# Kernel tuning notes

Hardware: AMD Instinct MI355X
Metric: run time of the kernel (lower is better)

The kernel has to match this reference:

```python
import jax, jax.numpy as jnp
import numpy as np

B, N, C = 64, 1024, 128
H1, H2 = 256, 128
ACTION = N


def _xavier(key, shape):
    lim = float(np.sqrt(6.0 / (shape[0] + shape[1])))
    return jax.random.uniform(key, shape, jnp.float32, -lim, lim)


def setup_inputs() -> dict:
    key = jax.random.key(0)
    ks = jax.random.split(key, 16)
    node_features = jax.random.normal(ks[0], (B, N, 3), jnp.float32)
    adjacency_matrix = jax.random.randint(ks[1], (B, N, N), 0, 2).astype(jnp.int32)
    return {
        "node_features": node_features,
        "adjacency_matrix": adjacency_matrix,
        "W_in": _xavier(ks[2], (3, C)),
        "a_src": _xavier(ks[3], (C, 1)),
        "a_dst": _xavier(ks[4], (C, 1)),
        "a_src2": _xavier(ks[5], (C, 1)),
        "a_dst2": _xavier(ks[6], (C, 1)),
        "W1": _xavier(ks[7], (C, H1)),
        "b1": jnp.zeros((H1,), jnp.float32),
        "W2": _xavier(ks[8], (H1, H2)),
        "b2": jnp.zeros((H2,), jnp.float32),
        "Wpi": _xavier(ks[9], (H2, ACTION)),
        "bpi": jnp.zeros((ACTION,), jnp.float32),
        "Wv": _xavier(ks[10], (H2, 1)),
        "bv": jnp.zeros((1,), jnp.float32),
    }


def _gat_layer(x, mask, a_src, a_dst):
    # x: [B,N,C]; mask: [B,N,N] bool
    ai = jnp.squeeze(x @ a_src, -1)  # [B,N] score of node as source (i)
    aj = jnp.squeeze(x @ a_dst, -1)  # [B,N] score of node as dest (j)
    e = ai[:, :, None] + aj[:, None, :]  # [B,N,N]
    e = jnp.where(e > 0, e, 0.2 * e)  # leaky_relu(0.2)
    e = jnp.where(mask, e, jnp.float32(-1e9))  # masked_fill(-inf)
    alpha = jax.nn.softmax(e, axis=-1)  # [B,N,N]
    out = jnp.einsum("bij,bjc->bic", alpha, x)  # weighted neighbor aggregation
    return jax.nn.relu(out)


def reference(node_features, adjacency_matrix, W_in, a_src, a_dst, a_src2, a_dst2,
              W1, b1, W2, b2, Wpi, bpi, Wv, bv):
    mask = adjacency_matrix > 0
    x = node_features @ W_in  # [B,N,C], no bias
    x = _gat_layer(x, mask, a_src, a_dst)
    x = _gat_layer(x, mask, a_src2, a_dst2)
    x = jnp.mean(x, axis=1)  # [B,C]
    x = jax.nn.relu(x @ W1 + b1)
    x = jax.nn.relu(x @ W2 + b2)
    pi = jax.nn.softmax(x @ Wpi + bpi, axis=1)
    v = x @ Wv + bv
    return (pi, v)
```

## Files before the change

### kernel.cpp

```cpp
#include <hip/hip_runtime.h>

#define Bn 64
#define Nn 1024
#define Cc 128

typedef _Float16 h8 __attribute__((ext_vector_type(8)));
typedef float f4v __attribute__((ext_vector_type(4)));
typedef unsigned long long u64;

__global__ __launch_bounds__(256) void k_feat(
    const float* __restrict__ nf, const float* __restrict__ Win,
    const float* __restrict__ asrc, const float* __restrict__ adst,
    _Float16* __restrict__ X0, float* __restrict__ ai, float* __restrict__ aj,
    float* __restrict__ E, float* __restrict__ G, float* __restrict__ F, float* __restrict__ H) {
  int g = blockIdx.x; int b = g >> 7; int n0 = (g & 127) << 3;
  int t = threadIdx.x; int c = t >> 1; int h = t & 1;
  __shared__ float sNf[24];
  if (t < 24) sNf[t] = nf[((size_t)(b << 10) + n0) * 3 + t];
  float w0 = Win[c], w1 = Win[Cc + c], w2 = Win[2 * Cc + c];
  float as_ = asrc[c], ad = adst[c];
  __syncthreads();
  float ps[4], pd[4];
  _Float16 hv[4];
  #pragma unroll
  for (int r = 0; r < 4; r++) {
    const float* p = sNf + ((h << 2) + r) * 3;
    float x = p[0] * w0 + p[1] * w1 + p[2] * w2;
    hv[r] = (_Float16)x; ps[r] = x * as_; pd[r] = x * ad;
  }
  *(uint2*)(X0 + ((size_t)b << 17) + ((size_t)(g & 127) << 10) + (c << 3) + (h << 2)) = *(uint2*)hv;
  #pragma unroll
  for (int off = 32; off > 1; off >>= 1) {
    #pragma unroll
    for (int r = 0; r < 4; r++) { ps[r] += __shfl_down(ps[r], off, 64); pd[r] += __shfl_down(pd[r], off, 64); }
  }
  __shared__ float red[4][2][4][2];
  int lane = t & 63, wv = t >> 6;
  if (lane < 2) {
    #pragma unroll
    for (int r = 0; r < 4; r++) { red[wv][lane][r][0] = ps[r]; red[wv][lane][r][1] = pd[r]; }
  }
  __syncthreads();
  if (t < 8) {
    int hh = t >> 2, r = t & 3;
    float sa = 0.f, sd = 0.f;
    #pragma unroll
    for (int w = 0; w < 4; w++) { sa += red[w][hh][r][0]; sd += red[w][hh][r][1]; }
    int gi = (b << 10) + n0 + t;
    ai[gi] = sa; aj[gi] = sd;
    E[gi] = __expf(sa); G[gi] = __expf(0.2f * sa);
    F[gi] = __expf(sd); H[gi] = __expf(0.2f * sd);
  }
}

template <int LAYER>
__global__ __launch_bounds__(256, 3) void k_agg(
    const _Float16* __restrict__ X, const int* __restrict__ adj,
    const float* __restrict__ ai, const float* __restrict__ E, const float* __restrict__ G,
    const float* __restrict__ aj, const float* __restrict__ F, const float* __restrict__ H,
    u64* __restrict__ pm, _Float16* __restrict__ Y, float* __restrict__ xmp,
    const float* __restrict__ as2, const float* __restrict__ ad2,
    float* __restrict__ ai2o, float* __restrict__ aj2o,
    float* __restrict__ E2o, float* __restrict__ G2o,
    float* __restrict__ F2o, float* __restrict__ H2o) {
  __shared__ __align__(16) char smem[34816];
  float* s_aj = (float*)smem;
  float* s_F  = (float*)(smem + 4096);
  float* s_H  = (float*)(smem + 8192);
  unsigned char* s_pm = (unsigned char*)(smem + 12288);
  float* tile = (float*)smem;
  float* s_as2 = (float*)(smem + 33792);
  float* s_ad2 = (float*)(smem + 34304);

  const int lin = blockIdx.x;
  const int b = lin & 63, tile_id = lin >> 6, i0 = tile_id << 6;
  const int tid = threadIdx.x;
  const int lane = tid & 63, wv = tid >> 6;
  const int m = lane & 15, quad = lane >> 4;
  const int wi = wv >> 1, wc = wv & 1;
  const int gbase = b << 10;

  ((float4*)s_aj)[tid] = ((const float4*)(aj + gbase))[tid];
  ((float4*)s_F)[tid]  = ((const float4*)(F + gbase))[tid];
  ((float4*)s_H)[tid]  = ((const float4*)(H + gbase))[tid];
  if (LAYER == 1 && tid < 128) { s_as2[tid] = as2[tid]; s_ad2[tid] = ad2[tid]; }

  if (LAYER == 1) {
    ushort* pmu = (ushort*)pm;
    #pragma unroll 2
    for (int pass = 0; pass < 16; ++pass) {
      int r = (wv << 4) + pass;
      const uint4* arow = (const uint4*)(adj + ((size_t)(gbase + i0 + r) << 10));
      uint4 v0 = arow[(lane << 2) | 0], v1 = arow[(lane << 2) | 1];
      uint4 v2 = arow[(lane << 2) | 2], v3 = arow[(lane << 2) | 3];
      unsigned int bits =
          (v0.x) | (v0.y << 1) | (v0.z << 2) | (v0.w << 3) |
          (v1.x << 4) | (v1.y << 5) | (v1.z << 6) | (v1.w << 7) |
          (v2.x << 8) | (v2.y << 9) | (v2.z << 10) | (v2.w << 11) |
          (v3.x << 12) | (v3.y << 13) | (v3.z << 14) | (v3.w << 15);
      *(ushort*)(s_pm + r * 152 + (lane << 1)) = (ushort)bits;
      pmu[((size_t)(gbase + i0 + r) << 6) + lane] = (ushort)bits;
    }
  } else {
    const u64* pmg = pm + (((size_t)(gbase + i0)) << 4);
    #pragma unroll
    for (int k = tid; k < 1024; k += 256) {
      int r = k >> 4, w = k & 15;
      *(u64*)(s_pm + r * 152 + (w << 3)) = pmg[k];
    }
  }

  const int r0 = (wi << 5) + m;
  const int gi0 = gbase + i0 + r0;
  const float ai0 = ai[gi0],      E0c = E[gi0],      G0c = G[gi0];
  const float ai1 = ai[gi0 + 16], E1c = E[gi0 + 16], G1c = G[gi0 + 16];
  float dsum0 = 0.f, dsum1 = 0.f;

  f4v acc[2][4];
  #pragma unroll
  for (int a = 0; a < 2; a++)
    #pragma unroll
    for (int ct = 0; ct < 4; ct++) { f4v z = {0.f, 0.f, 0.f, 0.f}; acc[a][ct] = z; }

  const char* gB = (const char*)(X + ((size_t)b << 17)) + (((quad << 7) + (wc << 6) + m) << 4);
  const unsigned char* pmr0 = s_pm + r0 * 152;
  const unsigned char* pmr1 = pmr0 + 16 * 152;

  auto LOADK = [&](int kt, h8& B0, h8& B1, h8& B2, h8& B3,
                   float4& W0, float4& W1, float4& Fw0, float4& Fw1,
                   float4& Hw0, float4& Hw1, unsigned& M0, unsigned& M1) {
    const char* gp = gB + ((size_t)kt << 13);
    B0 = *(const h8*)gp;          B1 = *(const h8*)(gp + 256);
    B2 = *(const h8*)(gp + 512);  B3 = *(const h8*)(gp + 768);
    const int j0 = (kt << 5) + (quad << 3);
    W0  = *(const float4*)&s_aj[j0]; W1  = *(const float4*)&s_aj[j0 + 4];
    Fw0 = *(const float4*)&s_F[j0];  Fw1 = *(const float4*)&s_F[j0 + 4];
    Hw0 = *(const float4*)&s_H[j0];  Hw1 = *(const float4*)&s_H[j0 + 4];
    M0 = pmr0[(kt << 2) + quad];     M1 = pmr1[(kt << 2) + quad];
  };
  auto COMP = [&](h8 B0, h8 B1, h8 B2, h8 B3,
                  float4 W0, float4 W1, float4 Fw0, float4 Fw1,
                  float4 Hw0, float4 Hw1, unsigned M0, unsigned M1) {
    float aw[8], fw[8], hw[8];
    *(float4*)&aw[0] = W0;  *(float4*)&aw[4] = W1;
    *(float4*)&fw[0] = Fw0; *(float4*)&fw[4] = Fw1;
    *(float4*)&hw[0] = Hw0; *(float4*)&hw[4] = Hw1;
    h8 a0, a1;
    #pragma unroll
    for (int e = 0; e < 8; e++) {
      float ew = aw[e], fe = fw[e], he = hw[e];
      bool p0 = (ai0 + ew) > 0.f;
      float v0 = (p0 ? E0c : G0c) * (p0 ? fe : he);
      v0 = ((M0 >> e) & 1u) ? v0 : 0.f;
      dsum0 += v0; a0[e] = (_Float16)v0;
      bool p1 = (ai1 + ew) > 0.f;
      float v1 = (p1 ? E1c : G1c) * (p1 ? fe : he);
      v1 = ((M1 >> e) & 1u) ? v1 : 0.f;
      dsum1 += v1; a1[e] = (_Float16)v1;
    }
    acc[0][0] = __builtin_amdgcn_mfma_f32_16x16x32_f16(a0, B0, acc[0][0], 0, 0, 0);
    acc[1][0] = __builtin_amdgcn_mfma_f32_16x16x32_f16(a1, B0, acc[1][0], 0, 0, 0);
    acc[0][1] = __builtin_amdgcn_mfma_f32_16x16x32_f16(a0, B1, acc[0][1], 0, 0, 0);
    acc[1][1] = __builtin_amdgcn_mfma_f32_16x16x32_f16(a1, B1, acc[1][1], 0, 0, 0);
    acc[0][2] = __builtin_amdgcn_mfma_f32_16x16x32_f16(a0, B2, acc[0][2], 0, 0, 0);
    acc[1][2] = __builtin_amdgcn_mfma_f32_16x16x32_f16(a1, B2, acc[1][2], 0, 0, 0);
    acc[0][3] = __builtin_amdgcn_mfma_f32_16x16x32_f16(a0, B3, acc[0][3], 0, 0, 0);
    acc[1][3] = __builtin_amdgcn_mfma_f32_16x16x32_f16(a1, B3, acc[1][3], 0, 0, 0);
  };

  __syncthreads();

  h8 Ab0, Ab1, Ab2, Ab3; float4 Aw0, Aw1, Af0, Af1, Ah0, Ah1; unsigned Am0, Am1;
  h8 Bb0, Bb1, Bb2, Bb3; float4 Bw0, Bw1, Bf0, Bf1, Bh0, Bh1; unsigned Bm0, Bm1;
  LOADK(0, Ab0, Ab1, Ab2, Ab3, Aw0, Aw1, Af0, Af1, Ah0, Ah1, Am0, Am1);
  for (int kt = 0; kt < 32; kt += 2) {
    LOADK(kt + 1, Bb0, Bb1, Bb2, Bb3, Bw0, Bw1, Bf0, Bf1, Bh0, Bh1, Bm0, Bm1);
    COMP(Ab0, Ab1, Ab2, Ab3, Aw0, Aw1, Af0, Af1, Ah0, Ah1, Am0, Am1);
    LOADK(kt + 2, Ab0, Ab1, Ab2, Ab3, Aw0, Aw1, Af0, Af1, Ah0, Ah1, Am0, Am1);
    COMP(Bb0, Bb1, Bb2, Bb3, Bw0, Bw1, Bf0, Bf1, Bh0, Bh1, Bm0, Bm1);
  }

  dsum0 += __shfl_xor(dsum0, 16, 64);
  dsum0 += __shfl_xor(dsum0, 32, 64);
  dsum1 += __shfl_xor(dsum1, 16, 64);
  dsum1 += __shfl_xor(dsum1, 32, 64);
  float rd8[2][4];
  #pragma unroll
  for (int r = 0; r < 4; r++) {
    int src = (quad << 2) + r;
    rd8[0][r] = 1.0f / __shfl(dsum0, src, 64);
    rd8[1][r] = 1.0f / __shfl(dsum1, src, 64);
  }

  __syncthreads();
  #pragma unroll
  for (int a = 0; a < 2; a++)
    #pragma unroll
    for (int ct = 0; ct < 4; ct++)
      #pragma unroll
      for (int r = 0; r < 4; r++) {
        int lr = (wi << 5) + (a << 4) + (quad << 2) + r;
        int c = (wc << 6) + (ct << 4) + m;
        tile[lr * 132 + c] = fmaxf(acc[a][ct][r] * rd8[a][r], 0.f);
      }
  __syncthreads();
  if (LAYER == 1) {
    _Float16 hv[32];
    #pragma unroll
    for (int s = 0; s < 32; s++) {
      int q = (tid << 5) + s;
      int li = ((q >> 10) << 3) + (q & 7), c = (q >> 3) & 127;
      hv[s] = (_Float16)tile[li * 132 + c];
    }
    uint4* o = (uint4*)(Y + ((size_t)b << 17) + ((size_t)i0 << 7) + (tid << 5));
    o[0] = *(uint4*)&hv[0]; o[1] = *(uint4*)&hv[8];
    o[2] = *(uint4*)&hv[16]; o[3] = *(uint4*)&hv[24];
    {
      int i = tid >> 2, p = tid & 3, cb = p << 5;
      const float* trow = tile + i * 132 + cb;
      float ssrc = 0.f, sdst = 0.f;
      #pragma unroll
      for (int k = 0; k < 32; k += 4) {
        float4 tv = *(const float4*)(trow + k);
        float4 av = *(const float4*)(s_as2 + cb + k);
        float4 dv = *(const float4*)(s_ad2 + cb + k);
        ssrc += tv.x * av.x + tv.y * av.y + tv.z * av.z + tv.w * av.w;
        sdst += tv.x * dv.x + tv.y * dv.y + tv.z * dv.z + tv.w * dv.w;
      }
      ssrc += __shfl_xor(ssrc, 1, 64); ssrc += __shfl_xor(ssrc, 2, 64);
      sdst += __shfl_xor(sdst, 1, 64); sdst += __shfl_xor(sdst, 2, 64);
      int gi = gbase + i0 + i;
      if (p == 0) { ai2o[gi] = ssrc; E2o[gi] = __expf(ssrc); G2o[gi] = __expf(0.2f * ssrc); }
      else if (p == 1) { aj2o[gi] = sdst; F2o[gi] = __expf(sdst); H2o[gi] = __expf(0.2f * sdst); }
    }
  } else {
    if (tid < 128) {
      float s = 0.f;
      #pragma unroll
      for (int i = 0; i < 64; i++) s += tile[i * 132 + tid];
      xmp[(((b << 4) + tile_id) << 7) + tid] = s;
    }
  }
}

__global__ __launch_bounds__(256) void k_head(
    const float* __restrict__ xmp, const float* __restrict__ W1, const float* __restrict__ b1,
    const float* __restrict__ W2, const float* __restrict__ b2,
    const float* __restrict__ Wpi, const float* __restrict__ bpi,
    const float* __restrict__ Wv, const float* __restrict__ bv,
    float* __restrict__ out) {
  int b = blockIdx.x, t = threadIdx.x;
  __shared__ float xs[128], h1[256], h2[128], red[4];
  if (t < 128) {
    const float* p = xmp + ((size_t)b << 11);
    float s = 0.f;
    #pragma unroll
    for (int xb = 0; xb < 16; xb++) s += p[(xb << 7) + t];
    xs[t] = s * (1.f / 1024.f);
  }
  __syncthreads();
  float s = 0.f;
  #pragma unroll 8
  for (int k = 0; k < 128; k++) s += xs[k] * W1[k * 256 + t];
  h1[t] = fmaxf(s + b1[t], 0.f);
  __syncthreads();
  if (t < 128) {
    float s2 = 0.f;
    #pragma unroll 8
    for (int k = 0; k < 256; k++) s2 += h1[k] * W2[k * 128 + t];
    h2[t] = fmaxf(s2 + b2[t], 0.f);
  }
  __syncthreads();
  float lg[4];
  #pragma unroll
  for (int q = 0; q < 4; q++) {
    int o = t + (q << 8);
    float s3 = 0.f;
    #pragma unroll 8
    for (int k = 0; k < 128; k++) s3 += h2[k] * Wpi[k * 1024 + o];
    lg[q] = s3 + bpi[o];
  }
  float mx = fmaxf(fmaxf(lg[0], lg[1]), fmaxf(lg[2], lg[3]));
  #pragma unroll
  for (int off = 32; off > 0; off >>= 1) mx = fmaxf(mx, __shfl_down(mx, off, 64));
  if ((t & 63) == 0) red[t >> 6] = mx;
  __syncthreads();
  mx = fmaxf(fmaxf(red[0], red[1]), fmaxf(red[2], red[3]));
  __syncthreads();
  float ex[4]; float sum = 0.f;
  #pragma unroll
  for (int q = 0; q < 4; q++) { ex[q] = __expf(lg[q] - mx); sum += ex[q]; }
  #pragma unroll
  for (int off = 32; off > 0; off >>= 1) sum += __shfl_down(sum, off, 64);
  if ((t & 63) == 0) red[t >> 6] = sum;
  __syncthreads();
  sum = red[0] + red[1] + red[2] + red[3];
  float rs = 1.0f / sum;
  #pragma unroll
  for (int q = 0; q < 4; q++) out[((size_t)b << 10) + t + (q << 8)] = ex[q] * rs;
  __syncthreads();
  float vp = (t < 128) ? h2[t] * Wv[t] : 0.f;
  #pragma unroll
  for (int off = 32; off > 0; off >>= 1) vp += __shfl_down(vp, off, 64);
  if ((t & 63) == 0) red[t >> 6] = vp;
  __syncthreads();
  if (t == 0) out[65536 + b] = red[0] + red[1] + red[2] + red[3] + bv[0];
}

extern "C" void kernel_launch(void* const* d_in, const int* in_sizes, int n_in,
                              void* d_out, int out_size, void* d_ws, size_t ws_size,
                              hipStream_t stream) {
  const float* nf    = (const float*)d_in[0];
  const int*   adj   = (const int*)  d_in[1];
  const float* Win   = (const float*)d_in[2];
  const float* asrc  = (const float*)d_in[3];
  const float* adst  = (const float*)d_in[4];
  const float* asrc2 = (const float*)d_in[5];
  const float* adst2 = (const float*)d_in[6];
  const float* W1    = (const float*)d_in[7];
  const float* b1    = (const float*)d_in[8];
  const float* W2    = (const float*)d_in[9];
  const float* b2    = (const float*)d_in[10];
  const float* Wpi   = (const float*)d_in[11];
  const float* bpi   = (const float*)d_in[12];
  const float* Wv    = (const float*)d_in[13];
  const float* bv    = (const float*)d_in[14];
  float* out = (float*)d_out;

  char* ws = (char*)d_ws;
  _Float16* x0 = (_Float16*)(ws);
  _Float16* x1 = (_Float16*)(ws + 16777216);
  u64* pm = (u64*)(ws + 33554432);
  char* S = ws + 41943040;
  float* ai1 = (float*)(S + 0 * 262144);
  float* aj1 = (float*)(S + 1 * 262144);
  float* E1  = (float*)(S + 2 * 262144);
  float* G1  = (float*)(S + 3 * 262144);
  float* F1  = (float*)(S + 4 * 262144);
  float* H1  = (float*)(S + 5 * 262144);
  float* ai2 = (float*)(S + 6 * 262144);
  float* aj2 = (float*)(S + 7 * 262144);
  float* E2  = (float*)(S + 8 * 262144);
  float* G2  = (float*)(S + 9 * 262144);
  float* F2  = (float*)(S + 10 * 262144);
  float* H2  = (float*)(S + 11 * 262144);
  float* xmp = (float*)(S + 12 * 262144);

  k_feat<<<8192, 256, 0, stream>>>(nf, Win, asrc, adst, x0, ai1, aj1, E1, G1, F1, H1);
  k_agg<1><<<1024, 256, 0, stream>>>(x0, adj, ai1, E1, G1, aj1, F1, H1, pm, x1, nullptr,
                                     asrc2, adst2, ai2, aj2, E2, G2, F2, H2);
  k_agg<2><<<1024, 256, 0, stream>>>(x1, nullptr, ai2, E2, G2, aj2, F2, H2, pm, nullptr, xmp,
                                     nullptr, nullptr, nullptr, nullptr, nullptr, nullptr, nullptr, nullptr);
  k_head<<<Bn, 256, 0, stream>>>(xmp, W1, b1, W2, b2, Wpi, bpi, Wv, bv, out);
}
```

Baseline: 564.6 us.

## Move adjacency bitpacking into feature kernel and simplify GAT softmax weights

Adjacency bit-packing moves out of layer-1 aggregation and into the feature kernel, which is much more parallel, so both aggregation layers now read the packed mask the same way. The leaky-relu branch is replaced by max(E*F, G*H), which is valid because exp is monotonic, so the ai/aj arrays and their comparisons are dropped. The mask is applied with bitwise AND on packed fp16 pairs. Row denominators are now computed with an extra MFMA against a ones vector instead of scalar sums and shuffles. Occupancy hint rises from 3 to 4 waves; risks include register pressure and fp16 rounding in the denominators.

Result: faster. 505.3 us (-10.5%).

```diff
diff --git a/kernel.cpp b/kernel.cpp
--- a/kernel.cpp
+++ b/kernel.cpp
@@ -5,16 +5,18 @@
 #define Cc 128
 
 typedef _Float16 h8 __attribute__((ext_vector_type(8)));
+typedef __fp16 fp16x2 __attribute__((ext_vector_type(2)));
 typedef float f4v __attribute__((ext_vector_type(4)));
 typedef unsigned long long u64;
 
 __global__ __launch_bounds__(256) void k_feat(
     const float* __restrict__ nf, const float* __restrict__ Win,
     const float* __restrict__ asrc, const float* __restrict__ adst,
-    _Float16* __restrict__ X0, float* __restrict__ ai, float* __restrict__ aj,
+    const int* __restrict__ adj, _Float16* __restrict__ X0, u64* __restrict__ pm,
     float* __restrict__ E, float* __restrict__ G, float* __restrict__ F, float* __restrict__ H) {
   int g = blockIdx.x; int b = g >> 7; int n0 = (g & 127) << 3;
   int t = threadIdx.x; int c = t >> 1; int h = t & 1;
+  int lane = t & 63, wv = t >> 6;
   __shared__ float sNf[24];
   if (t < 24) sNf[t] = nf[((size_t)(b << 10) + n0) * 3 + t];
   float w0 = Win[c], w1 = Win[Cc + c], w2 = Win[2 * Cc + c];
@@ -29,13 +31,31 @@
     hv[r] = (_Float16)x; ps[r] = x * as_; pd[r] = x * ad;
   }
   *(uint2*)(X0 + ((size_t)b << 17) + ((size_t)(g & 127) << 10) + (c << 3) + (h << 2)) = *(uint2*)hv;
+
+  {
+    ushort* pmu = (ushort*)pm;
+    int row = n0 + (wv << 1);
+    const uint4* ar = (const uint4*)(adj + (((size_t)(b << 10) + row) << 10));
+    #pragma unroll
+    for (int rr = 0; rr < 2; rr++) {
+      uint4 v0 = ar[(lane << 2) | 0], v1 = ar[(lane << 2) | 1];
+      uint4 v2 = ar[(lane << 2) | 2], v3 = ar[(lane << 2) | 3];
+      unsigned int bits =
+          (v0.x) | (v0.y << 1) | (v0.z << 2) | (v0.w << 3) |
+          (v1.x << 4) | (v1.y << 5) | (v1.z << 6) | (v1.w << 7) |
+          (v2.x << 8) | (v2.y << 9) | (v2.z << 10) | (v2.w << 11) |
+          (v3.x << 12) | (v3.y << 13) | (v3.z << 14) | (v3.w << 15);
+      pmu[(((size_t)(b << 10) + row + rr) << 6) + lane] = (ushort)bits;
+      ar += 256;
+    }
+  }
+
   #pragma unroll
   for (int off = 32; off > 1; off >>= 1) {
     #pragma unroll
     for (int r = 0; r < 4; r++) { ps[r] += __shfl_down(ps[r], off, 64); pd[r] += __shfl_down(pd[r], off, 64); }
   }
   __shared__ float red[4][2][4][2];
-  int lane = t & 63, wv = t >> 6;
   if (lane < 2) {
     #pragma unroll
     for (int r = 0; r < 4; r++) { red[wv][lane][r][0] = ps[r]; red[wv][lane][r][1] = pd[r]; }
@@ -47,27 +67,24 @@
     #pragma unroll
     for (int w = 0; w < 4; w++) { sa += red[w][hh][r][0]; sd += red[w][hh][r][1]; }
     int gi = (b << 10) + n0 + t;
-    ai[gi] = sa; aj[gi] = sd;
     E[gi] = __expf(sa); G[gi] = __expf(0.2f * sa);
     F[gi] = __expf(sd); H[gi] = __expf(0.2f * sd);
   }
 }
 
 template <int LAYER>
-__global__ __launch_bounds__(256, 3) void k_agg(
-    const _Float16* __restrict__ X, const int* __restrict__ adj,
-    const float* __restrict__ ai, const float* __restrict__ E, const float* __restrict__ G,
-    const float* __restrict__ aj, const float* __restrict__ F, const float* __restrict__ H,
-    u64* __restrict__ pm, _Float16* __restrict__ Y, float* __restrict__ xmp,
+__global__ __launch_bounds__(256, 4) void k_agg(
+    const _Float16* __restrict__ X,
+    const float* __restrict__ E, const float* __restrict__ G,
+    const float* __restrict__ F, const float* __restrict__ H,
+    const u64* __restrict__ pm, _Float16* __restrict__ Y, float* __restrict__ xmp,
     const float* __restrict__ as2, const float* __restrict__ ad2,
-    float* __restrict__ ai2o, float* __restrict__ aj2o,
     float* __restrict__ E2o, float* __restrict__ G2o,
     float* __restrict__ F2o, float* __restrict__ H2o) {
   __shared__ __align__(16) char smem[34816];
-  float* s_aj = (float*)smem;
-  float* s_F  = (float*)(smem + 4096);
-  float* s_H  = (float*)(smem + 8192);
-  unsigned char* s_pm = (unsigned char*)(smem + 12288);
+  float* s_F  = (float*)smem;
+  float* s_H  = (float*)(smem + 4096);
+  unsigned char* s_pm = (unsigned char*)(smem + 8192);
   float* tile = (float*)smem;
   float* s_as2 = (float*)(smem + 33792);
   float* s_ad2 = (float*)(smem + 34304);
@@ -80,117 +97,99 @@
   const int wi = wv >> 1, wc = wv & 1;
   const int gbase = b << 10;
 
-  ((float4*)s_aj)[tid] = ((const float4*)(aj + gbase))[tid];
-  ((float4*)s_F)[tid]  = ((const float4*)(F + gbase))[tid];
-  ((float4*)s_H)[tid]  = ((const float4*)(H + gbase))[tid];
-  if (LAYER == 1 && tid < 128) { s_as2[tid] = as2[tid]; s_ad2[tid] = ad2[tid]; }
-
-  if (LAYER == 1) {
-    ushort* pmu = (ushort*)pm;
-    #pragma unroll 2
-    for (int pass = 0; pass < 16; ++pass) {
-      int r = (wv << 4) + pass;
-      const uint4* arow = (const uint4*)(adj + ((size_t)(gbase + i0 + r) << 10));
-      uint4 v0 = arow[(lane << 2) | 0], v1 = arow[(lane << 2) | 1];
-      uint4 v2 = arow[(lane << 2) | 2], v3 = arow[(lane << 2) | 3];
-      unsigned int bits =
-          (v0.x) | (v0.y << 1) | (v0.z << 2) | (v0.w << 3) |
-          (v1.x << 4) | (v1.y << 5) | (v1.z << 6) | (v1.w << 7) |
-          (v2.x << 8) | (v2.y << 9) | (v2.z << 10) | (v2.w << 11) |
-          (v3.x << 12) | (v3.y << 13) | (v3.z << 14) | (v3.w << 15);
-      *(ushort*)(s_pm + r * 152 + (lane << 1)) = (ushort)bits;
-      pmu[((size_t)(gbase + i0 + r) << 6) + lane] = (ushort)bits;
-    }
-  } else {
-    const u64* pmg = pm + (((size_t)(gbase + i0)) << 4);
+  ((float4*)s_F)[tid] = ((const float4*)(F + gbase))[tid];
+  ((float4*)s_H)[tid] = ((const float4*)(H + gbase))[tid];
+  {
+    const u64* pmg = pm + ((size_t)(gbase + i0) << 4);
     #pragma unroll
     for (int k = tid; k < 1024; k += 256) {
       int r = k >> 4, w = k & 15;
       *(u64*)(s_pm + r * 152 + (w << 3)) = pmg[k];
     }
   }
+  if (LAYER == 1 && tid < 128) { s_as2[tid] = as2[tid]; s_ad2[tid] = ad2[tid]; }
 
   const int r0 = (wi << 5) + m;
   const int gi0 = gbase + i0 + r0;
-  const float ai0 = ai[gi0],      E0c = E[gi0],      G0c = G[gi0];
-  const float ai1 = ai[gi0 + 16], E1c = E[gi0 + 16], G1c = G[gi0 + 16];
-  float dsum0 = 0.f, dsum1 = 0.f;
+  const float E0c = E[gi0],      G0c = G[gi0];
+  const float E1c = E[gi0 + 16], G1c = G[gi0 + 16];
 
   f4v acc[2][4];
   #pragma unroll
   for (int a = 0; a < 2; a++)
     #pragma unroll
     for (int ct = 0; ct < 4; ct++) { f4v z = {0.f, 0.f, 0.f, 0.f}; acc[a][ct] = z; }
+  f4v accD0 = {0.f, 0.f, 0.f, 0.f}, accD1 = {0.f, 0.f, 0.f, 0.f};
+  const h8 kOne = {(_Float16)1.f, (_Float16)1.f, (_Float16)1.f, (_Float16)1.f,
+                   (_Float16)1.f, (_Float16)1.f, (_Float16)1.f, (_Float16)1.f};
 
   const char* gB = (const char*)(X + ((size_t)b << 17)) + (((quad << 7) + (wc << 6) + m) << 4);
   const unsigned char* pmr0 = s_pm + r0 * 152;
   const unsigned char* pmr1 = pmr0 + 16 * 152;
 
-  auto LOADK = [&](int kt, h8& B0, h8& B1, h8& B2, h8& B3,
-                   float4& W0, float4& W1, float4& Fw0, float4& Fw1,
-                   float4& Hw0, float4& Hw1, unsigned& M0, unsigned& M1) {
+  __syncthreads();
+
+  auto expand = [](unsigned mb, unsigned M[4]) {
+    unsigned slo = ((mb & 0xFu) * 0x204081u) & 0x01010101u;
+    unsigned shi = (((mb >> 4) & 0xFu) * 0x204081u) & 0x01010101u;
+    slo *= 0xFFu; shi *= 0xFFu;
+    M[0] = __builtin_amdgcn_perm(slo, slo, 0x01010000u);
+    M[1] = __builtin_amdgcn_perm(slo, slo, 0x03030202u);
+    M[2] = __builtin_amdgcn_perm(shi, shi, 0x01010000u);
+    M[3] = __builtin_amdgcn_perm(shi, shi, 0x03030202u);
+  };
+
+  auto LOADB = [&](int kt, h8* Bf, unsigned& mb0, unsigned& mb1) {
     const char* gp = gB + ((size_t)kt << 13);
-    B0 = *(const h8*)gp;          B1 = *(const h8*)(gp + 256);
-    B2 = *(const h8*)(gp + 512);  B3 = *(const h8*)(gp + 768);
+    Bf[0] = *(const h8*)gp;          Bf[1] = *(const h8*)(gp + 256);
+    Bf[2] = *(const h8*)(gp + 512);  Bf[3] = *(const h8*)(gp + 768);
+    mb0 = pmr0[(kt << 2) + quad];    mb1 = pmr1[(kt << 2) + quad];
+  };
+  auto COMP = [&](int kt, const h8* Bf, unsigned mb0, unsigned mb1) {
     const int j0 = (kt << 5) + (quad << 3);
-    W0  = *(const float4*)&s_aj[j0]; W1  = *(const float4*)&s_aj[j0 + 4];
-    Fw0 = *(const float4*)&s_F[j0];  Fw1 = *(const float4*)&s_F[j0 + 4];
-    Hw0 = *(const float4*)&s_H[j0];  Hw1 = *(const float4*)&s_H[j0 + 4];
-    M0 = pmr0[(kt << 2) + quad];     M1 = pmr1[(kt << 2) + quad];
+    float f[8], hh[8];
+    *(float4*)&f[0]  = *(const float4*)&s_F[j0]; *(float4*)&f[4]  = *(const float4*)&s_F[j0 + 4];
+    *(float4*)&hh[0] = *(const float4*)&s_H[j0]; *(float4*)&hh[4] = *(const float4*)&s_H[j0 + 4];
+    unsigned M0[4], M1[4];
+    expand(mb0, M0); expand(mb1, M1);
+    union { h8 v; unsigned u[4]; } A0, A1;
+    #pragma unroll
+    for (int q = 0; q < 4; q++) {
+      float u0 = fmaxf(E0c * f[2 * q], G0c * hh[2 * q]);
+      float u1 = fmaxf(E0c * f[2 * q + 1], G0c * hh[2 * q + 1]);
+      fp16x2 p0 = __builtin_amdgcn_cvt_pkrtz(u0, u1);
+      unsigned p0u; __builtin_memcpy(&p0u, &p0, 4);
+      A0.u[q] = p0u & M0[q];
+      float y0 = fmaxf(E1c * f[2 * q], G1c * hh[2 * q]);
+      float y1 = fmaxf(E1c * f[2 * q + 1], G1c * hh[2 * q + 1]);
+      fp16x2 p1 = __builtin_amdgcn_cvt_pkrtz(y0, y1);
+      unsigned p1u; __builtin_memcpy(&p1u, &p1, 4);
+      A1.u[q] = p1u & M1[q];
+    }
+    acc[0][0] = __builtin_amdgcn_mfma_f32_16x16x32_f16(A0.v, Bf[0], acc[0][0], 0, 0, 0);
+    acc[1][0] = __builtin_amdgcn_mfma_f32_16x16x32_f16(A1.v, Bf[0], acc[1][0], 0, 0, 0);
+    acc[0][1] = __builtin_amdgcn_mfma_f32_16x16x32_f16(A0.v, Bf[1], acc[0][1], 0, 0, 0);
+    acc[1][1] = __builtin_amdgcn_mfma_f32_16x16x32_f16(A1.v, Bf[1], acc[1][1], 0, 0, 0);
+    acc[0][2] = __builtin_amdgcn_mfma_f32_16x16x32_f16(A0.v, Bf[2], acc[0][2], 0, 0, 0);
+    acc[1][2] = __builtin_amdgcn_mfma_f32_16x16x32_f16(A1.v, Bf[2], acc[1][2], 0, 0, 0);
+    acc[0][3] = __builtin_amdgcn_mfma_f32_16x16x32_f16(A0.v, Bf[3], acc[0][3], 0, 0, 0);
+    acc[1][3] = __builtin_amdgcn_mfma_f32_16x16x32_f16(A1.v, Bf[3], acc[1][3], 0, 0, 0);
+    accD0 = __builtin_amdgcn_mfma_f32_16x16x32_f16(A0.v, kOne, accD0, 0, 0, 0);
+    accD1 = __builtin_amdgcn_mfma_f32_16x16x32_f16(A1.v, kOne, accD1, 0, 0, 0);
   };
-  auto COMP = [&](h8 B0, h8 B1, h8 B2, h8 B3,
-                  float4 W0, float4 W1, float4 Fw0, float4 Fw1,
-                  float4 Hw0, float4 Hw1, unsigned M0, unsigned M1) {
-    float aw[8], fw[8], hw[8];
-    *(float4*)&aw[0] = W0;  *(float4*)&aw[4] = W1;
-    *(float4*)&fw[0] = Fw0; *(float4*)&fw[4] = Fw1;
-    *(float4*)&hw[0] = Hw0; *(float4*)&hw[4] = Hw1;
-    h8 a0, a1;
-    #pragma unroll
-    for (int e = 0; e < 8; e++) {
-      float ew = aw[e], fe = fw[e], he = hw[e];
-      bool p0 = (ai0 + ew) > 0.f;
-      float v0 = (p0 ? E0c : G0c) * (p0 ? fe : he);
-      v0 = ((M0 >> e) & 1u) ? v0 : 0.f;
-      dsum0 += v0; a0[e] = (_Float16)v0;
-      bool p1 = (ai1 + ew) > 0.f;
-      float v1 = (p1 ? E1c : G1c) * (p1 ? fe : he);
-      v1 = ((M1 >> e) & 1u) ? v1 : 0.f;
-      dsum1 += v1; a1[e] = (_Float16)v1;
-    }
-    acc[0][0] = __builtin_amdgcn_mfma_f32_16x16x32_f16(a0, B0, acc[0][0], 0, 0, 0);
-    acc[1][0] = __builtin_amdgcn_mfma_f32_16x16x32_f16(a1, B0, acc[1][0], 0, 0, 0);
-    acc[0][1] = __builtin_amdgcn_mfma_f32_16x16x32_f16(a0, B1, acc[0][1], 0, 0, 0);
-    acc[1][1] = __builtin_amdgcn_mfma_f32_16x16x32_f16(a1, B1, acc[1][1], 0, 0, 0);
-    acc[0][2] = __builtin_amdgcn_mfma_f32_16x16x32_f16(a0, B2, acc[0][2], 0, 0, 0);
-    acc[1][2] = __builtin_amdgcn_mfma_f32_16x16x32_f16(a1, B2, acc[1][2], 0, 0, 0);
-    acc[0][3] = __builtin_amdgcn_mfma_f32_16x16x32_f16(a0, B3, acc[0][3], 0, 0, 0);
-    acc[1][3] = __builtin_amdgcn_mfma_f32_16x16x32_f16(a1, B3, acc[1][3], 0, 0, 0);
-  };
-
-  __syncthreads();
-
-  h8 Ab0, Ab1, Ab2, Ab3; float4 Aw0, Aw1, Af0, Af1, Ah0, Ah1; unsigned Am0, Am1;
-  h8 Bb0, Bb1, Bb2, Bb3; float4 Bw0, Bw1, Bf0, Bf1, Bh0, Bh1; unsigned Bm0, Bm1;
-  LOADK(0, Ab0, Ab1, Ab2, Ab3, Aw0, Aw1, Af0, Af1, Ah0, Ah1, Am0, Am1);
+
+  h8 Bf0[4], Bf1[4]; unsigned m00, m01, m10, m11;
+  LOADB(0, Bf0, m00, m01);
   for (int kt = 0; kt < 32; kt += 2) {
-    LOADK(kt + 1, Bb0, Bb1, Bb2, Bb3, Bw0, Bw1, Bf0, Bf1, Bh0, Bh1, Bm0, Bm1);
-    COMP(Ab0, Ab1, Ab2, Ab3, Aw0, Aw1, Af0, Af1, Ah0, Ah1, Am0, Am1);
-    LOADK(kt + 2, Ab0, Ab1, Ab2, Ab3, Aw0, Aw1, Af0, Af1, Ah0, Ah1, Am0, Am1);
-    COMP(Bb0, Bb1, Bb2, Bb3, Bw0, Bw1, Bf0, Bf1, Bh0, Bh1, Bm0, Bm1);
-  }
-
-  dsum0 += __shfl_xor(dsum0, 16, 64);
-  dsum0 += __shfl_xor(dsum0, 32, 64);
-  dsum1 += __shfl_xor(dsum1, 16, 64);
-  dsum1 += __shfl_xor(dsum1, 32, 64);
+    LOADB(kt + 1, Bf1, m10, m11);
+    COMP(kt, Bf0, m00, m01);
+    LOADB(kt + 2, Bf0, m00, m01);
+    COMP(kt + 1, Bf1, m10, m11);
+  }
+
   float rd8[2][4];
   #pragma unroll
-  for (int r = 0; r < 4; r++) {
-    int src = (quad << 2) + r;
-    rd8[0][r] = 1.0f / __shfl(dsum0, src, 64);
-    rd8[1][r] = 1.0f / __shfl(dsum1, src, 64);
-  }
+  for (int r = 0; r < 4; r++) { rd8[0][r] = 1.0f / accD0[r]; rd8[1][r] = 1.0f / accD1[r]; }
 
   __syncthreads();
   #pragma unroll
@@ -230,8 +229,8 @@
       ssrc += __shfl_xor(ssrc, 1, 64); ssrc += __shfl_xor(ssrc, 2, 64);
       sdst += __shfl_xor(sdst, 1, 64); sdst += __shfl_xor(sdst, 2, 64);
       int gi = gbase + i0 + i;
-      if (p == 0) { ai2o[gi] = ssrc; E2o[gi] = __expf(ssrc); G2o[gi] = __expf(0.2f * ssrc); }
-      else if (p == 1) { aj2o[gi] = sdst; F2o[gi] = __expf(sdst); H2o[gi] = __expf(0.2f * sdst); }
+      if (p == 0) { E2o[gi] = __expf(ssrc); G2o[gi] = __expf(0.2f * ssrc); }
+      else if (p == 1) { F2o[gi] = __expf(sdst); H2o[gi] = __expf(0.2f * sdst); }
     }
   } else {
     if (tid < 128) {
@@ -332,24 +331,20 @@
   _Float16* x1 = (_Float16*)(ws + 16777216);
   u64* pm = (u64*)(ws + 33554432);
   char* S = ws + 41943040;
-  float* ai1 = (float*)(S + 0 * 262144);
-  float* aj1 = (float*)(S + 1 * 262144);
   float* E1  = (float*)(S + 2 * 262144);
   float* G1  = (float*)(S + 3 * 262144);
   float* F1  = (float*)(S + 4 * 262144);
   float* H1  = (float*)(S + 5 * 262144);
-  float* ai2 = (float*)(S + 6 * 262144);
-  float* aj2 = (float*)(S + 7 * 262144);
   float* E2  = (float*)(S + 8 * 262144);
   float* G2  = (float*)(S + 9 * 262144);
   float* F2  = (float*)(S + 10 * 262144);
   float* H2  = (float*)(S + 11 * 262144);
   float* xmp = (float*)(S + 12 * 262144);
 
-  k_feat<<<8192, 256, 0, stream>>>(nf, Win, asrc, adst, x0, ai1, aj1, E1, G1, F1, H1);
-  k_agg<1><<<1024, 256, 0, stream>>>(x0, adj, ai1, E1, G1, aj1, F1, H1, pm, x1, nullptr,
-                                     asrc2, adst2, ai2, aj2, E2, G2, F2, H2);
-  k_agg<2><<<1024, 256, 0, stream>>>(x1, nullptr, ai2, E2, G2, aj2, F2, H2, pm, nullptr, xmp,
-                                     nullptr, nullptr, nullptr, nullptr, nullptr, nullptr, nullptr, nullptr);
+  k_feat<<<8192, 256, 0, stream>>>(nf, Win, asrc, adst, adj, x0, pm, E1, G1, F1, H1);
+  k_agg<1><<<1024, 256, 0, stream>>>(x0, E1, G1, F1, H1, pm, x1, nullptr,
+                                     asrc2, adst2, E2, G2, F2, H2);
+  k_agg<2><<<1024, 256, 0, stream>>>(x1, E2, G2, F2, H2, pm, nullptr, xmp,
+                                     nullptr, nullptr, nullptr, nullptr, nullptr, nullptr);
   k_head<<<Bn, 256, 0, stream>>>(xmp, W1, b1, W2, b2, Wpi, bpi, Wv, bv, out);
 }
```
